# Kernel tuning notes

Hardware: AMD Instinct MI355X
Metric: run time of the kernel (lower is better)

## Reference

```python
import jax, jax.numpy as jnp
import numpy as np
import math

NB = 4           # num_bands
EPS = 1e-5       # LayerNorm eps


def _dwconv(x, w):
    # depthwise Conv1d, padding=1, kernel=3. x: [b, t, c], w: [c, 1, k]
    c = x.shape[-1]
    y = jax.lax.conv_general_dilated(
        x.transpose(0, 2, 1), w, window_strides=(1,), padding=[(1, 1)],
        dimension_numbers=('NCH', 'OIH', 'NCH'), feature_group_count=c)
    return y.transpose(0, 2, 1)


def _ln(x, g, b):
    m = jnp.mean(x, axis=-1, keepdims=True)
    v = jnp.mean(jnp.square(x - m), axis=-1, keepdims=True)
    return (x - m) * jax.lax.rsqrt(v + EPS) * g + b


def _attn(x, mem, qw, qc, kw, kc, vw, vc, ow, pw, prev_qk):
    # x, mem: [b, w, c]
    b, w, c = x.shape
    d = c // NB
    q = _dwconv(x @ qw.T, qc).reshape(b, w, NB, d).transpose(0, 2, 1, 3)      # [b,nb,w,d]
    k = _dwconv(mem @ kw.T, kc).reshape(b, w, NB, d).transpose(0, 2, 3, 1)    # [b,nb,d,w]
    v = _dwconv(mem @ vw.T, vc).reshape(b, w, NB, d).transpose(0, 2, 1, 3)    # [b,nb,w,d]
    # skewed relative-position bias: matmul + pad + transpose + slice
    p = jnp.einsum('bnwd,dt->bnwt', q, pw[:, :w])                              # [b,nb,w,w]
    p = jnp.pad(p, ((0, 0), (0, 0), (0, 0), (1, 0)))                           # pad last dim left
    p = p.transpose(0, 1, 3, 2)[:, :, 1:, :]                                   # skew
    qk = (jnp.einsum('bnwd,bndt->bnwt', q, k) + p) / math.sqrt(c)
    if prev_qk is not None:
        qk = qk + prev_qk
    a = jnp.einsum('bnwt,bntd->bnwd', jax.nn.softmax(qk, axis=-1), v)
    a = a.transpose(0, 2, 1, 3).reshape(b, w, c)
    return a @ ow.T, qk


def setup_inputs() -> dict:
    key = jax.random.key(0)
    ks = jax.random.split(key, 32)
    B, CH, BINS, W, FF = 4, 8, 1024, 1024, 2048
    s = 0.02
    inp = {
        'x': jax.random.normal(ks[0], (B, CH, BINS, W), jnp.float32),
        'mem': jax.random.normal(ks[1], (B, CH, BINS, W), jnp.float32),
        'prev_qk1': jax.random.normal(ks[2], (B, NB, W, W), jnp.float32),
        'prev_qk2': jax.random.normal(ks[3], (B, NB, W, W), jnp.float32),
        'ip_w': jax.random.normal(ks[4], (CH,), jnp.float32) * s,
        'ip_b': jnp.zeros((1,), jnp.float32),
        'mp_w': jax.random.normal(ks[5], (CH,), jnp.float32) * s,
        'mp_b': jnp.zeros((1,), jnp.float32),
        'ln1_g': jnp.ones((BINS,), jnp.float32), 'ln1_b': jnp.zeros((BINS,), jnp.float32),
        'ln2_g': jnp.ones((BINS,), jnp.float32), 'ln2_b': jnp.zeros((BINS,), jnp.float32),
        'ln3_g': jnp.ones((BINS,), jnp.float32), 'ln3_b': jnp.zeros((BINS,), jnp.float32),
        'a1_qw': jax.random.normal(ks[6], (BINS, BINS), jnp.float32) * s,
        'a1_qc': jax.random.normal(ks[7], (BINS, 1, 3), jnp.float32) * 0.3,
        'a1_kw': jax.random.normal(ks[8], (BINS, BINS), jnp.float32) * s,
        'a1_kc': jax.random.normal(ks[9], (BINS, 1, 3), jnp.float32) * 0.3,
        'a1_vw': jax.random.normal(ks[10], (BINS, BINS), jnp.float32) * s,
        'a1_vc': jax.random.normal(ks[11], (BINS, 1, 3), jnp.float32) * 0.3,
        'a1_ow': jax.random.normal(ks[12], (BINS, BINS), jnp.float32) * s,
        'a1_pw': jax.random.normal(ks[13], (BINS // NB, W), jnp.float32),
        'a2_qw': jax.random.normal(ks[14], (BINS, BINS), jnp.float32) * s,
        'a2_qc': jax.random.normal(ks[15], (BINS, 1, 3), jnp.float32) * 0.3,
        'a2_kw': jax.random.normal(ks[16], (BINS, BINS), jnp.float32) * s,
        'a2_kc': jax.random.normal(ks[17], (BINS, 1, 3), jnp.float32) * 0.3,
        'a2_vw': jax.random.normal(ks[18], (BINS, BINS), jnp.float32) * s,
        'a2_vc': jax.random.normal(ks[19], (BINS, 1, 3), jnp.float32) * 0.3,
        'a2_ow': jax.random.normal(ks[20], (BINS, BINS), jnp.float32) * s,
        'a2_pw': jax.random.normal(ks[21], (BINS // NB, W), jnp.float32),
        'l1_w': jax.random.normal(ks[22], (FF, BINS), jnp.float32) * s,
        'l2_w': jax.random.normal(ks[23], (BINS, FF), jnp.float32) * s,
    }
    return inp


def reference(x, mem, prev_qk1, prev_qk2, ip_w, ip_b, mp_w, mp_b,
              ln1_g, ln1_b, ln2_g, ln2_b, ln3_g, ln3_b,
              a1_qw, a1_qc, a1_kw, a1_kc, a1_vw, a1_vc, a1_ow, a1_pw,
              a2_qw, a2_qc, a2_kw, a2_kc, a2_vw, a2_vc, a2_ow, a2_pw,
              l1_w, l2_w):
    # 1x1 Conv2d to 1 channel then [b, w, bins] layout
    xs = jnp.einsum('bchw,c->bwh', x, ip_w) + ip_b    # [b, w, bins]
    ms = jnp.einsum('bchw,c->bwh', mem, mp_w) + mp_b
    # self-attention with prev_qk residual
    h, qk1 = _attn(_ln(xs, ln1_g, ln1_b), _ln(xs, ln1_g, ln1_b),
                   a1_qw, a1_qc, a1_kw, a1_kc, a1_vw, a1_vc, a1_ow, a1_pw, prev_qk1)
    xs = xs + h
    # cross-attention against mem
    h, qk2 = _attn(_ln(xs, ln2_g, ln2_b), ms,
                   a2_qw, a2_qc, a2_kw, a2_kc, a2_vw, a2_vc, a2_ow, a2_pw, prev_qk2)
    xs = xs + h
    # squared-ReLU FFN
    h = _ln(xs, ln3_g, ln3_b)
    h = jnp.square(jax.nn.relu(h @ l1_w.T)) @ l2_w.T
    xs = xs + h
    out = xs.transpose(0, 2, 1)[:, None]              # [b, 1, bins, w]
    return (out, qk1, qk2)
```

## Files before the change

kernel.cpp:

```cpp
#include <hip/hip_runtime.h>
#include <stdint.h>

typedef unsigned short u16;
typedef __bf16 bfv8 __attribute__((ext_vector_type(8)));
typedef float f32x4 __attribute__((ext_vector_type(4)));
typedef unsigned short u16x8 __attribute__((ext_vector_type(8)));

#define DI __device__ __forceinline__

DI u16 f2bf(float f) {
  union { float f; unsigned u; } c; c.f = f;
  unsigned r = c.u + 0x7FFFu + ((c.u >> 16) & 1u);
  return (u16)(r >> 16);
}
DI float bf2f(u16 b) {
  union { unsigned u; float f; } c; c.u = ((unsigned)b) << 16;
  return c.f;
}

enum { EPI_BF16 = 0, EPI_RELU2 = 1, EPI_ADDF32 = 2, EPI_QK = 3, EPI_TOUT = 4 };

#define GLDS(g, l)                                                              \
  __builtin_amdgcn_global_load_lds((const __attribute__((address_space(1))) void*)(g), \
                                   (__attribute__((address_space(3))) void*)(l), 16, 0, 0)

#define VMCNT_BAR(N)                                        \
  do {                                                      \
    asm volatile("s_waitcnt vmcnt(" #N ")" ::: "memory");   \
    __builtin_amdgcn_sched_barrier(0);                      \
    __builtin_amdgcn_s_barrier();                           \
    __builtin_amdgcn_sched_barrier(0);                      \
  } while (0)

#define BAR_ONLY()                                          \
  do {                                                      \
    __builtin_amdgcn_sched_barrier(0);                      \
    __builtin_amdgcn_s_barrier();                           \
    __builtin_amdgcn_sched_barrier(0);                      \
  } while (0)

template <int EPI, bool KSPLIT>
__global__ __launch_bounds__(512, 4) void gemm128(
    const u16* __restrict__ Aq, const u16* __restrict__ Akv, int asplit,
    long a1q, long a1r, int lda1,
    const u16* __restrict__ A2, int lda2,
    const u16* __restrict__ B1, long b1q, long b1r, int ldb1,
    const u16* __restrict__ B2, long b2q, long b2r, int ldb2,
    int K, int ksp,
    void* __restrict__ Cv, long cq, long cr, int ldc,
    const float* __restrict__ extra, long eq, int lde,
    float scale)
{
  constexpr int SS = 16384;
  __shared__ __align__(16) u16 lds[2 * SS];
  const int tid = threadIdx.x;
  const int wid = tid >> 6, lane = tid & 63;

  const int gx = gridDim.x, gy = gridDim.y;
  const int nwg = gx * gy * (int)gridDim.z;
  const int flat = blockIdx.x + gx * (blockIdx.y + gy * blockIdx.z);
  const int q = nwg >> 3, r = nwg & 7;
  const int xcd = flat & 7, idx = flat >> 3;
  const int wg = (xcd < r ? xcd * (q + 1) : r * (q + 1) + (xcd - r) * q) + idx;
  const int bx = wg % gx;
  const int tmp = wg / gx;
  const int by = tmp % gy;
  const int bz = tmp / gy;

  const long zq = bz >> 2, zr = bz & 3;
  const int m0 = by * 128, n0 = bx * 128;
  const u16* Ab = ((n0 >= asplit) ? Akv : Aq) + zq * a1q + zr * a1r;
  const u16* Bb = B1 + zq * b1q + zr * b1r;
  const u16* B2b = KSPLIT ? (B2 + zq * b2q + zr * b2r) : (const u16*)nullptr;
  const int wm = (wid >> 2) * 64, wn = (wid & 3) * 32;
  const int fr = lane & 15, fq = lane >> 4;

  f32x4 acc[4][2];
#pragma unroll
  for (int i = 0; i < 4; ++i)
#pragma unroll
    for (int j = 0; j < 2; ++j)
      acc[i][j] = (f32x4){0.f, 0.f, 0.f, 0.f};

  const int nt = K >> 6;

  auto STAGE = [&](int tt, int sb) {
    const int k0 = tt << 6;
    u16* Ld = &lds[sb * SS];
    const u16* Asrc; int la; const u16* Bsrc; int lb;
    if (!KSPLIT || k0 < ksp) { Asrc = Ab + k0; la = lda1; Bsrc = Bb + k0; lb = ldb1; }
    else { Asrc = A2 + (k0 - ksp); la = lda2; Bsrc = B2b + (k0 - ksp); lb = ldb2; }
#pragma unroll
    for (int l = 0; l < 2; ++l) {
      int idx2 = (l << 9) + tid;
      int row = idx2 >> 3;
      int sc = ((idx2 & 7) ^ (row & 7)) << 3;
      GLDS(Asrc + (size_t)(m0 + row) * la + sc,
           Ld + (((l << 3) + wid) << 9));
    }
#pragma unroll
    for (int l = 0; l < 2; ++l) {
      int idx2 = (l << 9) + tid;
      int row = idx2 >> 3;
      int sc = ((idx2 & 7) ^ (row & 7)) << 3;
      GLDS(Bsrc + (size_t)(n0 + row) * lb + sc,
           Ld + 8192 + (((l << 3) + wid) << 9));
    }
  };

  auto COMPUTE = [&](int cb) {
    const u16* As = &lds[cb * SS];
    const u16* Bs = As + 8192;
#pragma unroll
    for (int ks = 0; ks < 2; ++ks) {
      bfv8 av[4];
#pragma unroll
      for (int i = 0; i < 4; ++i) {
        int ra = wm + i * 16 + fr;
        int ca = (((ks << 2) + fq) ^ (ra & 7)) << 3;
        av[i] = *(const bfv8*)&As[(ra << 6) + ca];
      }
      bfv8 bv[2];
#pragma unroll
      for (int j = 0; j < 2; ++j) {
        int rb = wn + (j << 4) + fr;
        int cb2 = (((ks << 2) + fq) ^ (rb & 7)) << 3;
        bv[j] = *(const bfv8*)&Bs[(rb << 6) + cb2];
      }
      __builtin_amdgcn_s_setprio(1);
#pragma unroll
      for (int i = 0; i < 4; ++i) {
        acc[i][0] = __builtin_amdgcn_mfma_f32_16x16x32_bf16(av[i], bv[0], acc[i][0], 0, 0, 0);
        acc[i][1] = __builtin_amdgcn_mfma_f32_16x16x32_bf16(av[i], bv[1], acc[i][1], 0, 0, 0);
      }
      __builtin_amdgcn_s_setprio(0);
    }
  };

  STAGE(0, 0);
  STAGE(1, 1);
  VMCNT_BAR(4);
  for (int t = 0; t < nt; ++t) {
    COMPUTE(t & 1);
    BAR_ONLY();
    if (t + 2 < nt) {
      STAGE(t + 2, t & 1);
      VMCNT_BAR(4);
    } else if (t + 1 < nt) {
      VMCNT_BAR(0);
    }
  }

  if constexpr (EPI == EPI_BF16 || EPI == EPI_RELU2) {
    u16* Cb = (u16*)Cv + zq * cq + zr * cr;
#pragma unroll
    for (int i = 0; i < 4; ++i)
#pragma unroll
      for (int j = 0; j < 2; ++j)
#pragma unroll
        for (int r2 = 0; r2 < 4; ++r2) {
          int row = m0 + wm + i * 16 + (fq << 2) + r2;
          int col = n0 + wn + j * 16 + fr;
          float v = acc[i][j][r2];
          if constexpr (EPI == EPI_RELU2) { v = fmaxf(v, 0.f); v = v * v; }
          Cb[(size_t)row * ldc + col] = f2bf(v);
        }
  } else if constexpr (EPI == EPI_ADDF32) {
    float* Cb = (float*)Cv + zq * cq + zr * cr;
#pragma unroll
    for (int i = 0; i < 4; ++i)
#pragma unroll
      for (int j = 0; j < 2; ++j)
#pragma unroll
        for (int r2 = 0; r2 < 4; ++r2) {
          int row = m0 + wm + i * 16 + (fq << 2) + r2;
          int col = n0 + wn + j * 16 + fr;
          Cb[(size_t)row * ldc + col] += acc[i][j][r2];
        }
  } else if constexpr (EPI == EPI_TOUT) {
    float* Ob = (float*)Cv;
    const float* Xb = extra;
#pragma unroll
    for (int i = 0; i < 4; ++i)
#pragma unroll
      for (int j = 0; j < 2; ++j)
#pragma unroll
        for (int r2 = 0; r2 < 4; ++r2) {
          int row = m0 + wm + i * 16 + (fq << 2) + r2;
          int col = n0 + wn + j * 16 + fr;
          float v = Xb[(size_t)row * lde + col] + acc[i][j][r2];
          Ob[(((size_t)(row >> 10) << 10) + col) * 1024 + (row & 1023)] = v;
        }
  } else {
    float* Cb = (float*)Cv + zq * cq + zr * cr;
    const float* Eb = extra + (size_t)bz * eq;
#pragma unroll
    for (int i = 0; i < 4; ++i)
#pragma unroll
      for (int j = 0; j < 2; ++j)
#pragma unroll
        for (int r2 = 0; r2 < 4; ++r2) {
          int row = m0 + wm + i * 16 + (fq << 2) + r2;
          int col = n0 + wn + j * 16 + fr;
          Cb[(size_t)row * ldc + col] = acc[i][j][r2] * scale + Eb[(size_t)row * lde + col];
        }
  }
}

__global__ __launch_bounds__(256) void proj4_kernel(const float* __restrict__ x,
                                                    const float* __restrict__ memp,
                                                    const float* __restrict__ ipw,
                                                    const float* __restrict__ ipb,
                                                    const float* __restrict__ mpw,
                                                    const float* __restrict__ mpb,
                                                    float* __restrict__ xs,
                                                    u16* __restrict__ msb)
{
  __shared__ __align__(16) float sbuf[2][16][256];
  const int t = threadIdx.x;
  const int wid = t >> 6, lane = t & 63;
  const int task = blockIdx.z >> 2;
  const int b = blockIdx.z & 3;
  const int h0 = blockIdx.x << 4;
  const int w0 = blockIdx.y << 8;
  const float* src = task ? memp : x;
  const float* w8 = task ? mpw : ipw;
  const float bias = task ? mpb[0] : ipb[0];
  const int crot = (blockIdx.x + blockIdx.y + blockIdx.z) & 7;
  float wr[8];
#pragma unroll
  for (int j = 0; j < 8; ++j) wr[j] = w8[(j + crot) & 7];
  float acc[16];
#pragma unroll
  for (int h = 0; h < 16; ++h) acc[h] = bias;
  const size_t bbase = ((size_t)b * 8) << 20;

  auto STAGE_C = [&](int i, int sb) {
    const int c = (i + crot) & 7;
    const float* g = src + bbase + ((size_t)c << 20) + (size_t)h0 * 1024 + w0 + (lane << 2);
#pragma unroll
    for (int l = 0; l < 4; ++l) {
      int row = (wid << 2) + l;
      GLDS(g + (size_t)row * 1024, &sbuf[sb][row][0]);
    }
  };

  STAGE_C(0, 0);
  STAGE_C(1, 1);
#pragma unroll
  for (int i = 0; i < 8; ++i) {
    if (i < 7) VMCNT_BAR(4); else VMCNT_BAR(0);
    {
      const float wc = wr[i];
      const int sb = i & 1;
#pragma unroll
      for (int h = 0; h < 16; ++h)
        acc[h] += sbuf[sb][h][t] * wc;
    }
    BAR_ONLY();
    if (i + 2 < 8) STAGE_C(i + 2, i & 1);
  }

  if (task) {
    u16* d = &msb[((size_t)b * 1024 + w0 + t) * 1024 + h0];
    u16x8 o0, o1;
#pragma unroll
    for (int h = 0; h < 8; ++h) { o0[h] = f2bf(acc[h]); o1[h] = f2bf(acc[h + 8]); }
    *(u16x8*)&d[0] = o0;
    *(u16x8*)&d[8] = o1;
  } else {
    float* d = &xs[((size_t)b * 1024 + w0 + t) * 1024 + h0];
#pragma unroll
    for (int p = 0; p < 4; ++p) {
      f32x4 v = {acc[p * 4], acc[p * 4 + 1], acc[p * 4 + 2], acc[p * 4 + 3]};
      *(f32x4*)&d[p * 4] = v;
    }
  }
}

__global__ __launch_bounds__(256) void ln_kernel(const float* __restrict__ x,
                                                 const float* __restrict__ g,
                                                 const float* __restrict__ b,
                                                 u16* __restrict__ out)
{
  int row = blockIdx.x, tid = threadIdx.x;
  float4 v = ((const float4*)(x + (size_t)row * 1024))[tid];
  float s = v.x + v.y + v.z + v.w;
  float s2 = v.x * v.x + v.y * v.y + v.z * v.z + v.w * v.w;
#pragma unroll
  for (int o = 32; o; o >>= 1) { s += __shfl_down(s, o); s2 += __shfl_down(s2, o); }
  __shared__ float rs[4], rs2[4];
  int wid = tid >> 6, lane = tid & 63;
  if (lane == 0) { rs[wid] = s; rs2[wid] = s2; }
  __syncthreads();
  s = rs[0] + rs[1] + rs[2] + rs[3];
  s2 = rs2[0] + rs2[1] + rs2[2] + rs2[3];
  float mean = s * (1.f / 1024.f);
  float var = s2 * (1.f / 1024.f) - mean * mean;
  float rstd = rsqrtf(var + 1e-5f);
  float4 gv = ((const float4*)g)[tid];
  float4 bv = ((const float4*)b)[tid];
  ushort4 o;
  o.x = f2bf((v.x - mean) * rstd * gv.x + bv.x);
  o.y = f2bf((v.y - mean) * rstd * gv.y + bv.y);
  o.z = f2bf((v.z - mean) * rstd * gv.z + bv.z);
  o.w = f2bf((v.w - mean) * rstd * gv.w + bv.w);
  ((ushort4*)out)[(size_t)row * 256 + tid] = o;
}

__global__ __launch_bounds__(128) void dwconv_qk_kernel(const u16* __restrict__ qkv,
                                                        const float* __restrict__ qc,
                                                        const float* __restrict__ kc,
                                                        u16* __restrict__ Qc,
                                                        u16* __restrict__ Kc)
{
  int sel = blockIdx.y;
  int row = blockIdx.x;
  int t = row & 1023;
  int c0 = threadIdx.x * 8;
  const u16* r0 = qkv + (size_t)row * 3072 + (sel << 10) + c0;
  const float* wc = sel ? kc : qc;
  u16* dst = (sel ? Kc : Qc) + (size_t)row * 1024 + c0;
  u16x8 zv = {0, 0, 0, 0, 0, 0, 0, 0};
  u16x8 xm = zv, xp = zv;
  if (t > 0) xm = *(const u16x8*)(r0 - 3072);
  u16x8 xc = *(const u16x8*)r0;
  if (t < 1023) xp = *(const u16x8*)(r0 + 3072);
  u16x8 o;
#pragma unroll
  for (int j = 0; j < 8; ++j) {
    int c = c0 + j;
    float v = bf2f(xm[j]) * wc[c * 3 + 0] + bf2f(xc[j]) * wc[c * 3 + 1] + bf2f(xp[j]) * wc[c * 3 + 2];
    o[j] = f2bf(v);
  }
  *(u16x8*)dst = o;
}

__global__ __launch_bounds__(1024) void dwconv_t_kernel(const u16* __restrict__ qkv,
                                                        const float* __restrict__ wc,
                                                        u16* __restrict__ out)
{
  __shared__ float tile[32][33];
  int b = blockIdx.z;
  int t = blockIdx.x * 32 + threadIdx.y;
  int c = blockIdx.y * 32 + threadIdx.x;
  size_t base = ((size_t)b * 1024 + t) * 3072 + 2048 + c;
  float xm = (t > 0) ? bf2f(qkv[base - 3072]) : 0.f;
  float xc = bf2f(qkv[base]);
  float xp = (t < 1023) ? bf2f(qkv[base + 3072]) : 0.f;
  tile[threadIdx.y][threadIdx.x] = xm * wc[c * 3 + 0] + xc * wc[c * 3 + 1] + xp * wc[c * 3 + 2];
  __syncthreads();
  int c2 = blockIdx.y * 32 + threadIdx.y;
  int t2 = blockIdx.x * 32 + threadIdx.x;
  int z = b * 4 + (c2 >> 8);
  out[((size_t)z * 256 + (c2 & 255)) * 1024 + t2] = f2bf(tile[threadIdx.x][threadIdx.y]);
}

__global__ __launch_bounds__(1024) void softmax_kernel(const float* __restrict__ qk,
                                                       u16* __restrict__ P)
{
  const int wv = threadIdx.x >> 6, lane = threadIdx.x & 63;
  const size_t row = (size_t)blockIdx.x * 16 + wv;
  const float* src = &qk[row * 1024];
  f32x4 v[4];
#pragma unroll
  for (int i = 0; i < 4; ++i) v[i] = *(const f32x4*)&src[i * 256 + lane * 4];
  float m = v[0].x;
#pragma unroll
  for (int i = 0; i < 4; ++i)
    m = fmaxf(m, fmaxf(fmaxf(v[i].x, v[i].y), fmaxf(v[i].z, v[i].w)));
#pragma unroll
  for (int o = 32; o; o >>= 1) m = fmaxf(m, __shfl_xor(m, o));
  float e[4][4];
  float s = 0.f;
#pragma unroll
  for (int i = 0; i < 4; ++i) {
    e[i][0] = __expf(v[i].x - m); e[i][1] = __expf(v[i].y - m);
    e[i][2] = __expf(v[i].z - m); e[i][3] = __expf(v[i].w - m);
    s += e[i][0] + e[i][1] + e[i][2] + e[i][3];
  }
#pragma unroll
  for (int o = 32; o; o >>= 1) s += __shfl_xor(s, o);
  float rinv = 1.f / s;
  u16* dst = &P[row * 1024];
#pragma unroll
  for (int i = 0; i < 4; ++i) {
    ushort4 o;
    o.x = f2bf(e[i][0] * rinv); o.y = f2bf(e[i][1] * rinv);
    o.z = f2bf(e[i][2] * rinv); o.w = f2bf(e[i][3] * rinv);
    *(ushort4*)&dst[i * 256 + lane * 4] = o;
  }
}

struct CastJobs { const float* s[12]; u16* d[12]; };
__global__ __launch_bounds__(256) void cast12_kernel(CastJobs J)
{
  int j = blockIdx.y;
  int i = blockIdx.x * 256 + threadIdx.x;
  float4 v = ((const float4*)J.s[j])[i];
  ushort4 o;
  o.x = f2bf(v.x); o.y = f2bf(v.y); o.z = f2bf(v.z); o.w = f2bf(v.w);
  ((ushort4*)J.d[j])[i] = o;
}

__global__ __launch_bounds__(1024) void pwt_kernel(const float* __restrict__ pw,
                                                   u16* __restrict__ pwT)
{
  __shared__ float tile[32][33];
  int d = blockIdx.y * 32 + threadIdx.y;
  int t = blockIdx.x * 32 + threadIdx.x;
  tile[threadIdx.y][threadIdx.x] = pw[(size_t)d * 1024 + t];
  __syncthreads();
  int t2 = blockIdx.x * 32 + threadIdx.y;
  int d2 = blockIdx.y * 32 + threadIdx.x;
  pwT[(size_t)t2 * 256 + d2] = f2bf(tile[threadIdx.x][threadIdx.y]);
}

static void run_attn(hipStream_t stream, float* xs, const u16* qsrc, const u16* kvsrc, int asplit,
                     u16* QKVraw, u16* Qc, u16* Kc, u16* Vt, u16* P, u16* Am,
                     const u16* wqkv, const u16* wo, const u16* pwt,
                     const float* qc, const float* kc, const float* vc,
                     const float* prevqk, float* qko)
{
  dim3 blk(512);
  gemm128<EPI_BF16, false><<<dim3(24, 32, 1), blk, 0, stream>>>(
      qsrc, kvsrc, asplit, 0, 0, 1024, nullptr, 0,
      wqkv, 0, 0, 1024, nullptr, 0, 0, 0,
      1024, 0, QKVraw, 0, 0, 3072, nullptr, 0, 0, 1.f);
  dwconv_qk_kernel<<<dim3(4096, 2), 128, 0, stream>>>(QKVraw, qc, kc, Qc, Kc);
  dwconv_t_kernel<<<dim3(32, 32, 4), dim3(32, 32), 0, stream>>>(QKVraw, vc, Vt);
  gemm128<EPI_QK, true><<<dim3(8, 8, 16), blk, 0, stream>>>(
      Qc, Qc, 1 << 30, 1048576, 256, 1024, pwt, 256,
      Kc, 1048576, 256, 1024, Qc, 1048576, 256, 1024,
      512, 256, qko, 4194304, 1048576, 1024, prevqk, 1048576, 1024, 0.03125f);
  softmax_kernel<<<1024, 1024, 0, stream>>>(qko, P);
  gemm128<EPI_BF16, false><<<dim3(2, 8, 16), blk, 0, stream>>>(
      P, P, 1 << 30, 4194304, 1048576, 1024, nullptr, 0,
      Vt, 1048576, 262144, 1024, nullptr, 0, 0, 0,
      1024, 0, Am, 1048576, 256, 1024, nullptr, 0, 0, 1.f);
  gemm128<EPI_ADDF32, false><<<dim3(8, 32, 1), blk, 0, stream>>>(
      Am, Am, 1 << 30, 0, 0, 1024, nullptr, 0,
      wo, 0, 0, 1024, nullptr, 0, 0, 0,
      1024, 0, xs, 0, 0, 1024, nullptr, 0, 0, 1.f);
}

extern "C" void kernel_launch(void* const* d_in, const int* in_sizes, int n_in,
                              void* d_out, int out_size, void* d_ws, size_t ws_size,
                              hipStream_t stream)
{
  (void)in_sizes; (void)n_in; (void)out_size; (void)ws_size;
  const float* x    = (const float*)d_in[0];
  const float* memp = (const float*)d_in[1];
  const float* pqk1 = (const float*)d_in[2];
  const float* pqk2 = (const float*)d_in[3];
  const float* ip_w = (const float*)d_in[4];
  const float* ip_b = (const float*)d_in[5];
  const float* mp_w = (const float*)d_in[6];
  const float* mp_b = (const float*)d_in[7];
  const float* ln1g = (const float*)d_in[8];
  const float* ln1b = (const float*)d_in[9];
  const float* ln2g = (const float*)d_in[10];
  const float* ln2b = (const float*)d_in[11];
  const float* ln3g = (const float*)d_in[12];
  const float* ln3b = (const float*)d_in[13];
  const float* a1qw = (const float*)d_in[14];
  const float* a1qc = (const float*)d_in[15];
  const float* a1kw = (const float*)d_in[16];
  const float* a1kc = (const float*)d_in[17];
  const float* a1vw = (const float*)d_in[18];
  const float* a1vc = (const float*)d_in[19];
  const float* a1ow = (const float*)d_in[20];
  const float* a1pw = (const float*)d_in[21];
  const float* a2qw = (const float*)d_in[22];
  const float* a2qc = (const float*)d_in[23];
  const float* a2kw = (const float*)d_in[24];
  const float* a2kc = (const float*)d_in[25];
  const float* a2vw = (const float*)d_in[26];
  const float* a2vc = (const float*)d_in[27];
  const float* a2ow = (const float*)d_in[28];
  const float* a2pw = (const float*)d_in[29];
  const float* l1w  = (const float*)d_in[30];
  const float* l2w  = (const float*)d_in[31];

  float* outp = (float*)d_out;
  float* qk1o = outp + 4194304;
  float* qk2o = outp + 20971520;

  const size_t MB = 1024 * 1024;
  char* W = (char*)d_ws;
  float* xs   = (float*)(W);
  u16* msb    = (u16*)(W + 16 * MB);
  u16* xln    = (u16*)(W + 24 * MB);
  u16* QKVraw = (u16*)(W + 32 * MB);
  u16* Qc     = (u16*)(W + 56 * MB);
  u16* Kc     = (u16*)(W + 64 * MB);
  u16* Vt     = (u16*)(W + 72 * MB);
  u16* P      = (u16*)(W + 80 * MB);
  u16* Am     = (u16*)(W + 112 * MB);
  u16* wqkv1  = (u16*)(W + 120 * MB);
  u16* wqkv2  = (u16*)(W + 126 * MB);
  u16* wo1    = (u16*)(W + 132 * MB);
  u16* wo2    = (u16*)(W + 134 * MB);
  u16* wl1    = (u16*)(W + 136 * MB);
  u16* wl2    = (u16*)(W + 140 * MB);
  u16* pwt1   = (u16*)(W + 144 * MB);
  u16* pwt2   = (u16*)(W + 144 * MB + 512 * 1024);
  u16* H1     = QKVraw;

  CastJobs J;
  J.s[0] = a1qw; J.d[0] = wqkv1;
  J.s[1] = a1kw; J.d[1] = wqkv1 + 1048576;
  J.s[2] = a1vw; J.d[2] = wqkv1 + 2097152;
  J.s[3] = a2qw; J.d[3] = wqkv2;
  J.s[4] = a2kw; J.d[4] = wqkv2 + 1048576;
  J.s[5] = a2vw; J.d[5] = wqkv2 + 2097152;
  J.s[6] = a1ow; J.d[6] = wo1;
  J.s[7] = a2ow; J.d[7] = wo2;
  J.s[8] = l1w;            J.d[8] = wl1;
  J.s[9] = l1w + 1048576;  J.d[9] = wl1 + 1048576;
  J.s[10] = l2w;           J.d[10] = wl2;
  J.s[11] = l2w + 1048576; J.d[11] = wl2 + 1048576;
  cast12_kernel<<<dim3(1024, 12), 256, 0, stream>>>(J);
  pwt_kernel<<<dim3(32, 8, 1), dim3(32, 32), 0, stream>>>(a1pw, pwt1);
  pwt_kernel<<<dim3(32, 8, 1), dim3(32, 32), 0, stream>>>(a2pw, pwt2);

  proj4_kernel<<<dim3(64, 4, 8), 256, 0, stream>>>(
      x, memp, ip_w, ip_b, mp_w, mp_b, xs, msb);

  ln_kernel<<<4096, 256, 0, stream>>>(xs, ln1g, ln1b, xln);
  run_attn(stream, xs, xln, xln, 1 << 30, QKVraw, Qc, Kc, Vt, P, Am,
           wqkv1, wo1, pwt1, a1qc, a1kc, a1vc, pqk1, qk1o);

  ln_kernel<<<4096, 256, 0, stream>>>(xs, ln2g, ln2b, xln);
  run_attn(stream, xs, xln, msb, 1024, QKVraw, Qc, Kc, Vt, P, Am,
           wqkv2, wo2, pwt2, a2qc, a2kc, a2vc, pqk2, qk2o);

  ln_kernel<<<4096, 256, 0, stream>>>(xs, ln3g, ln3b, xln);
  gemm128<EPI_RELU2, false><<<dim3(16, 32, 1), dim3(512), 0, stream>>>(
      xln, xln, 1 << 30, 0, 0, 1024, nullptr, 0,
      wl1, 0, 0, 1024, nullptr, 0, 0, 0,
      1024, 0, H1, 0, 0, 2048, nullptr, 0, 0, 1.f);
  gemm128<EPI_TOUT, false><<<dim3(8, 32, 1), dim3(512), 0, stream>>>(
      H1, H1, 1 << 30, 0, 0, 2048, nullptr, 0,
      wl2, 0, 0, 2048, nullptr, 0, 0, 0,
      2048, 0, outp, 0, 0, 1024, xs, 0, 1024, 1.f);
}
```

Baseline: 463.6 us.

## Add dedicated 256x256-tile QK score kernel with pipelined LDS staging

Replaces the generic 128-tile GEMM used for the attention scores plus skewed position bias with a specialized kernel. Each block computes a 256x256 output tile as four 128x128 quadrants over a concatenated K of 512 (Q·K plus the position-bias term). Loads are staged half-tile at a time into double-buffered, XOR-swizzled LDS, interleaved with MFMA phases, and blocks are remapped so consecutive blocks are spread across z. The goal is more operand reuse per block and better overlap of loads with compute, at the cost of 128KB of LDS, fewer blocks (256) and higher register pressure.

New measurement: 468.3 us. No clear change (+1.0%).

```diff
diff --git a/kernel.cpp b/kernel.cpp
--- a/kernel.cpp
+++ b/kernel.cpp
@@ -205,6 +205,114 @@
           Cb[(size_t)row * ldc + col] = acc[i][j][r2] * scale + Eb[(size_t)row * lde + col];
         }
   }
+}
+
+__global__ __launch_bounds__(512) void qk8_kernel(
+    const u16* __restrict__ Qc, const u16* __restrict__ Kc,
+    const u16* __restrict__ pwt, const float* __restrict__ prev,
+    float* __restrict__ out)
+{
+  __shared__ __align__(16) u16 lds[65536];
+  const int tid = threadIdx.x;
+  const int wid = tid >> 6, lane = tid & 63;
+  const int flat = blockIdx.x + 4 * (blockIdx.y + 4 * blockIdx.z);
+  const int wg = (flat & 7) * 32 + (flat >> 3);
+  const int bx = wg & 3, by = (wg >> 2) & 3, z = wg >> 4;
+  const int m0 = by * 256, n0 = bx * 256;
+  const u16* Qz = Qc + ((size_t)(z >> 2) << 20) + ((z & 3) << 8);
+  const u16* Kz = Kc + ((size_t)(z >> 2) << 20) + ((z & 3) << 8);
+  const int mrow = (wid >> 2) * 64;
+  const int ncol = (wid & 3) * 32;
+  const int fr = lane & 15, fq = lane >> 4;
+
+  f32x4 acc[2][2][4][2];
+#pragma unroll
+  for (int a = 0; a < 2; ++a)
+#pragma unroll
+    for (int b = 0; b < 2; ++b)
+#pragma unroll
+      for (int i = 0; i < 4; ++i)
+#pragma unroll
+        for (int j = 0; j < 2; ++j)
+          acc[a][b][i][j] = (f32x4){0.f, 0.f, 0.f, 0.f};
+
+  auto SH = [&](int w, int mat, int h) {
+    const int k0 = w << 6;
+    u16* dst = lds + ((w & 1) << 15) + (mat << 14) + (h << 13);
+    const u16* src; int ld;
+    if (k0 < 256) { src = (mat ? Kz : Qz) + k0; ld = 1024; }
+    else { src = mat ? (Qz + (k0 - 256)) : (pwt + (k0 - 256)); ld = mat ? 1024 : 256; }
+    const int base = (mat ? n0 : m0) + (h << 7);
+#pragma unroll
+    for (int l = 0; l < 2; ++l) {
+      int idx2 = (l << 9) + tid;
+      int r = idx2 >> 3;
+      int sc = ((idx2 & 7) ^ (r & 7)) << 3;
+      GLDS(src + (size_t)(base + r) * ld + sc, dst + (((l << 3) + wid) << 9));
+    }
+  };
+
+#define QK8_PHASE(AA, BB, STG)                                                   \
+  {                                                                              \
+    bfv8 av[4][2], bv[2][2];                                                     \
+    _Pragma("unroll") for (int i = 0; i < 4; ++i) {                              \
+      int R = (AA) * 128 + mrow + i * 16 + fr;                                   \
+      _Pragma("unroll") for (int ks = 0; ks < 2; ++ks)                           \
+        av[i][ks] = *(const bfv8*)&Ac[(R << 6) + ((((ks << 2) + fq) ^ (R & 7)) << 3)]; \
+    }                                                                            \
+    _Pragma("unroll") for (int j = 0; j < 2; ++j) {                              \
+      int R = (BB) * 128 + ncol + j * 16 + fr;                                   \
+      _Pragma("unroll") for (int ks = 0; ks < 2; ++ks)                           \
+        bv[j][ks] = *(const bfv8*)&Bc[(R << 6) + ((((ks << 2) + fq) ^ (R & 7)) << 3)]; \
+    }                                                                            \
+    STG;                                                                         \
+    BAR_ONLY();                                                                  \
+    asm volatile("s_waitcnt lgkmcnt(0)" ::: "memory");                           \
+    __builtin_amdgcn_sched_barrier(0);                                           \
+    __builtin_amdgcn_s_setprio(1);                                               \
+    _Pragma("unroll") for (int ks = 0; ks < 2; ++ks)                             \
+      _Pragma("unroll") for (int i = 0; i < 4; ++i)                              \
+        _Pragma("unroll") for (int j = 0; j < 2; ++j)                            \
+          acc[AA][BB][i][j] = __builtin_amdgcn_mfma_f32_16x16x32_bf16(           \
+              av[i][ks], bv[j][ks], acc[AA][BB][i][j], 0, 0, 0);                 \
+    __builtin_amdgcn_s_setprio(0);                                               \
+  }
+
+  SH(0, 0, 0); SH(0, 0, 1); SH(0, 1, 0); SH(0, 1, 1);
+  SH(1, 0, 0); SH(1, 1, 0);
+  VMCNT_BAR(4);
+
+  for (int v = 0; v < 8; ++v) {
+    const u16* Ac = lds + ((v & 1) << 15);
+    const u16* Bc = Ac + 16384;
+    QK8_PHASE(0, 0, { if (v + 1 < 8) { SH(v + 1, 0, 1); SH(v + 1, 1, 1); } });
+    BAR_ONLY();
+    QK8_PHASE(0, 1, {});
+    BAR_ONLY();
+    QK8_PHASE(1, 0, { if (v + 2 < 8) SH(v + 2, 0, 0); });
+    BAR_ONLY();
+    QK8_PHASE(1, 1, { if (v + 2 < 8) SH(v + 2, 1, 0); });
+    VMCNT_BAR(4);
+  }
+#undef QK8_PHASE
+
+  float* Co = out + ((size_t)z << 20);
+  const float* Eo = prev + ((size_t)z << 20);
+#pragma unroll
+  for (int a = 0; a < 2; ++a)
+#pragma unroll
+    for (int b = 0; b < 2; ++b)
+#pragma unroll
+      for (int i = 0; i < 4; ++i)
+#pragma unroll
+        for (int j = 0; j < 2; ++j)
+#pragma unroll
+          for (int r2 = 0; r2 < 4; ++r2) {
+            int row = m0 + a * 128 + mrow + i * 16 + (fq << 2) + r2;
+            int col = n0 + b * 128 + ncol + j * 16 + fr;
+            Co[(size_t)row * 1024 + col] =
+                acc[a][b][i][j][r2] * 0.03125f + Eo[(size_t)row * 1024 + col];
+          }
 }
 
 __global__ __launch_bounds__(256) void proj4_kernel(const float* __restrict__ x,
@@ -429,10 +537,7 @@
       1024, 0, QKVraw, 0, 0, 3072, nullptr, 0, 0, 1.f);
   dwconv_qk_kernel<<<dim3(4096, 2), 128, 0, stream>>>(QKVraw, qc, kc, Qc, Kc);
   dwconv_t_kernel<<<dim3(32, 32, 4), dim3(32, 32), 0, stream>>>(QKVraw, vc, Vt);
-  gemm128<EPI_QK, true><<<dim3(8, 8, 16), blk, 0, stream>>>(
-      Qc, Qc, 1 << 30, 1048576, 256, 1024, pwt, 256,
-      Kc, 1048576, 256, 1024, Qc, 1048576, 256, 1024,
-      512, 256, qko, 4194304, 1048576, 1024, prevqk, 1048576, 1024, 0.03125f);
+  qk8_kernel<<<dim3(4, 4, 16), blk, 0, stream>>>(Qc, Kc, pwt, prevqk, qko);
   softmax_kernel<<<1024, 1024, 0, stream>>>(qko, P);
   gemm128<EPI_BF16, false><<<dim3(2, 8, 16), blk, 0, stream>>>(
       P, P, 1 << 30, 4194304, 1048576, 1024, nullptr, 0,
```
